# Kernel tuning notes

Measured on AMD Instinct MI355X. Metric: run time of the kernel, lower is better.

The kernel has to match this reference:

```python
import jax, jax.numpy as jnp
import numpy as np

N, E, F_IN, F_EXP, H, C = 8192, 65536, 3247, 7993, 3, 512
HC = H * C
NEG_SLOPE = 0.2


def setup_inputs() -> dict:
    key = jax.random.key(0)
    ks = jax.random.split(key, 40)
    s = 0.02
    rnd = lambda k, *sh: (jax.random.normal(k, sh, jnp.float32) * s)
    d = {}
    d['x'] = jax.random.normal(ks[0], (N, F_IN), jnp.float32)
    d['edge_index'] = jax.random.randint(ks[1], (2, E), 0, N, jnp.int32)
    d['exp'] = jax.random.normal(ks[2], (N, F_EXP), jnp.float32)
    # GATv2 layer 1 (in=3247)
    d['w1l'] = rnd(ks[3], F_IN, HC); d['b1l'] = rnd(ks[4], HC)
    d['w1r'] = rnd(ks[5], F_IN, HC); d['b1r'] = rnd(ks[6], HC)
    d['a1'] = rnd(ks[7], H, C);      d['o1'] = rnd(ks[8], HC)
    # GATv2 layer 2 (in=1536)
    d['w2l'] = rnd(ks[9], HC, HC);  d['b2l'] = rnd(ks[10], HC)
    d['w2r'] = rnd(ks[11], HC, HC); d['b2r'] = rnd(ks[12], HC)
    d['a2'] = rnd(ks[13], H, C);     d['o2'] = rnd(ks[14], HC)
    # GATv2 layer 3 (in=1536)
    d['w3l'] = rnd(ks[15], HC, HC); d['b3l'] = rnd(ks[16], HC)
    d['w3r'] = rnd(ks[17], HC, HC); d['b3r'] = rnd(ks[18], HC)
    d['a3'] = rnd(ks[19], H, C);     d['o3'] = rnd(ks[20], HC)
    # encoder: 7993 -> 4000 -> 1500 -> 512
    d['e1w'] = rnd(ks[21], F_EXP, 4000); d['e1b'] = rnd(ks[22], 4000)
    d['e2w'] = rnd(ks[23], 4000, 1500);  d['e2b'] = rnd(ks[24], 1500)
    d['e3w'] = rnd(ks[25], 1500, 512);   d['e3b'] = rnd(ks[26], 512)
    # head: 2048 -> 1024 -> 512 -> 1
    d['l1w'] = rnd(ks[27], HC + 512, 1024); d['l1b'] = rnd(ks[28], 1024)
    d['l2w'] = rnd(ks[29], 1024, 512);      d['l2b'] = rnd(ks[30], 512)
    d['l3w'] = rnd(ks[31], 512, 1);         d['l3b'] = rnd(ks[32], 1)
    return d


def gatv2(h, src, dst, wl, bl, wr, br, att, out_bias):
    # PyG GATv2Conv: e_ij = a^T LeakyReLU(W_l h_j + W_r h_i), softmax over j per target i,
    # out_i = sum_j alpha_ij * (W_l h_j), concat heads, + bias.
    xl = (h @ wl + bl).reshape(N, H, C)
    xr = (h @ wr + br).reshape(N, H, C)
    e = jax.nn.leaky_relu(xl[src] + xr[dst], NEG_SLOPE)      # [E', H, C]
    logit = jnp.einsum('ehc,hc->eh', e, att)                  # [E', H]
    m = jax.ops.segment_max(logit, dst, num_segments=N)       # [N, H]
    p = jnp.exp(logit - m[dst])
    z = jax.ops.segment_sum(p, dst, num_segments=N)
    alpha = p / z[dst]                                        # segment softmax
    out = jax.ops.segment_sum(alpha[:, :, None] * xl[src], dst, num_segments=N)
    return out.reshape(N, HC) + out_bias


def reference(x, edge_index, exp,
              w1l, b1l, w1r, b1r, a1, o1,
              w2l, b2l, w2r, b2r, a2, o2,
              w3l, b3l, w3r, b3r, a3, o3,
              e1w, e1b, e2w, e2b, e3w, e3b,
              l1w, l1b, l2w, l2b, l3w, l3b):
    loops = jnp.arange(N, dtype=edge_index.dtype)
    src = jnp.concatenate([edge_index[0], loops])  # add_self_loops=True (PyG default)
    dst = jnp.concatenate([edge_index[1], loops])
    h = jax.nn.relu(gatv2(x, src, dst, w1l, b1l, w1r, b1r, a1, o1))
    h = jax.nn.relu(gatv2(h, src, dst, w2l, b2l, w2r, b2r, a2, o2))
    h = jax.nn.relu(gatv2(h, src, dst, w3l, b3l, w3r, b3r, a3, o3))
    cell = jax.nn.relu(exp @ e1w + e1b)
    cell = jax.nn.relu(cell @ e2w + e2b)
    cell = cell @ e3w + e3b
    z = jnp.concatenate([h, cell], axis=1)  # [N, 2048]
    z = jax.nn.relu(z @ l1w + l1b)
    z = jax.nn.relu(z @ l2w + l2b)
    return z @ l3w + l3b  # [N, 1]
```

## Files before the change

kernel.cpp:

```cpp
#include <hip/hip_runtime.h>
#include <stdint.h>

#define NN 8192
#define NE 65536
#define ET (NE + NN)
#define F_IN   3247
#define F_IN_P 3264
#define F_EXP   7993
#define F_EXP_P 8000

typedef __attribute__((ext_vector_type(8))) short bf16x8;
typedef __attribute__((ext_vector_type(4))) float f32x4;

typedef const __attribute__((address_space(1))) void gvoid_t;
typedef __attribute__((address_space(3))) void lvoid_t;

__device__ __forceinline__ float bf2f(uint16_t u) {
  union { uint32_t i; float f; } v; v.i = ((uint32_t)u) << 16; return v.f;
}
__device__ __forceinline__ uint16_t f2bf(float f) {
  union { float f; uint32_t i; } v; v.f = f;
  uint32_t r = v.i + 0x7fffu + ((v.i >> 16) & 1u);
  return (uint16_t)(r >> 16);
}

__device__ __forceinline__ void gld_lds16(const void* g, void* l) {
  __builtin_amdgcn_global_load_lds((gvoid_t*)g, (lvoid_t*)l, 16, 0, 0);
}

#define BARRIER() do { __builtin_amdgcn_sched_barrier(0); \
                       __builtin_amdgcn_s_barrier(); \
                       __builtin_amdgcn_sched_barrier(0); } while (0)
#define LGKM0()   do { asm volatile("s_waitcnt lgkmcnt(0)" ::: "memory"); \
                       __builtin_amdgcn_sched_barrier(0); } while (0)

__device__ __forceinline__ void stage4(const char* src, char* dst, size_t Kb) {
#pragma unroll
  for (int j = 0; j < 4; ++j)
    gld_lds16(src + (size_t)(j * 64) * Kb, dst + j * 8192);
}

__global__ __launch_bounds__(512, 2)
void gemm256(const uint16_t* __restrict__ A, const uint16_t* __restrict__ Bt,
             const float* __restrict__ bias, int biasN, int relu,
             uint16_t* __restrict__ C, int Kp, int ldc, int nbn)
{
  extern __shared__ char smem[];
  const int tid = threadIdx.x;
  const int w = tid >> 6, lane = tid & 63;
  const int wr = w >> 2, wc = w & 3;
  const int fr = lane & 15, g = lane >> 4;

  const int nwg = (int)gridDim.x;
  const int id = (int)blockIdx.x;
  const int q = nwg >> 3, r = nwg & 7;
  const int xcd = id & 7, idx = id >> 3;
  const int wg = (xcd < r ? xcd * (q + 1) : r * (q + 1) + (xcd - r) * q) + idx;
  const int brow = (wg / nbn) * 256, bcol = (wg % nbn) * 256;

  const size_t Kb = (size_t)Kp * 2;

  const int srow = tid >> 3;
  const int sswz = ((tid & 7) ^ (srow & 7)) * 16;
  const char* pA = (const char*)A + (size_t)(brow + srow) * Kb + sswz;
  const char* pB = (const char*)Bt + (size_t)(bcol + srow) * Kb + sswz;
  char* sA = smem + w * 1024;
  char* sB = smem + 65536 + w * 1024;

  const int sw0 = ((g) ^ (fr & 7)) * 16;
  const int sw1 = ((g + 4) ^ (fr & 7)) * 16;
  const int arow = (wr * 128 + fr) * 128;
  const int brow_o = (wc * 64 + fr) * 128;

  f32x4 acc[8][4];
#pragma unroll
  for (int m = 0; m < 8; ++m)
#pragma unroll
    for (int n = 0; n < 4; ++n) acc[m][n] = (f32x4){0.f, 0.f, 0.f, 0.f};
  bf16x8 af[8][2], bg[4][2];

  stage4(pA, sA, Kb);
  stage4(pB, sB, Kb);
  stage4(pA + 128, sA + 32768, Kb);
  stage4(pB + 128, sB + 32768, Kb);
  asm volatile("s_waitcnt vmcnt(8)" ::: "memory");
  BARRIER();

  const int nk = Kp >> 6;
  for (int t = 0; t < nk; ++t) {
    const int buf = (t & 1) << 15;
    const char* aB = smem + buf + arow;
    const char* bB = smem + 65536 + buf + brow_o;

#pragma unroll
    for (int m = 0; m < 4; ++m) {
      af[m][0] = *(const bf16x8*)(aB + m * 2048 + sw0);
      af[m][1] = *(const bf16x8*)(aB + m * 2048 + sw1);
    }
#pragma unroll
    for (int n = 0; n < 2; ++n) {
      bg[n][0] = *(const bf16x8*)(bB + n * 2048 + sw0);
      bg[n][1] = *(const bf16x8*)(bB + n * 2048 + sw1);
    }
    BARRIER(); LGKM0();
    __builtin_amdgcn_s_setprio(1);
#pragma unroll
    for (int m = 0; m < 4; ++m)
#pragma unroll
      for (int n = 0; n < 2; ++n) {
        acc[m][n] = __builtin_amdgcn_mfma_f32_16x16x32_bf16(af[m][0], bg[n][0], acc[m][n], 0, 0, 0);
        acc[m][n] = __builtin_amdgcn_mfma_f32_16x16x32_bf16(af[m][1], bg[n][1], acc[m][n], 0, 0, 0);
      }
    __builtin_amdgcn_s_setprio(0);
    BARRIER();

#pragma unroll
    for (int m = 4; m < 8; ++m) {
      af[m][0] = *(const bf16x8*)(aB + m * 2048 + sw0);
      af[m][1] = *(const bf16x8*)(aB + m * 2048 + sw1);
    }
#pragma unroll
    for (int n = 2; n < 4; ++n) {
      bg[n][0] = *(const bf16x8*)(bB + n * 2048 + sw0);
      bg[n][1] = *(const bf16x8*)(bB + n * 2048 + sw1);
    }
    BARRIER(); LGKM0();
    __builtin_amdgcn_s_setprio(1);
#pragma unroll
    for (int m = 4; m < 8; ++m)
#pragma unroll
      for (int n = 0; n < 2; ++n) {
        acc[m][n] = __builtin_amdgcn_mfma_f32_16x16x32_bf16(af[m][0], bg[n][0], acc[m][n], 0, 0, 0);
        acc[m][n] = __builtin_amdgcn_mfma_f32_16x16x32_bf16(af[m][1], bg[n][1], acc[m][n], 0, 0, 0);
      }
    __builtin_amdgcn_s_setprio(0);
    BARRIER();

    if (t + 2 < nk) stage4(pA + (size_t)(t + 2) * 128, sA + (((t + 2) & 1) << 15), Kb);
    BARRIER();
    __builtin_amdgcn_s_setprio(1);
#pragma unroll
    for (int m = 0; m < 4; ++m)
#pragma unroll
      for (int n = 2; n < 4; ++n) {
        acc[m][n] = __builtin_amdgcn_mfma_f32_16x16x32_bf16(af[m][0], bg[n][0], acc[m][n], 0, 0, 0);
        acc[m][n] = __builtin_amdgcn_mfma_f32_16x16x32_bf16(af[m][1], bg[n][1], acc[m][n], 0, 0, 0);
      }
    __builtin_amdgcn_s_setprio(0);
    BARRIER();

    if (t + 2 < nk) stage4(pB + (size_t)(t + 2) * 128, sB + (((t + 2) & 1) << 15), Kb);
    BARRIER();
    __builtin_amdgcn_s_setprio(1);
#pragma unroll
    for (int m = 4; m < 8; ++m)
#pragma unroll
      for (int n = 2; n < 4; ++n) {
        acc[m][n] = __builtin_amdgcn_mfma_f32_16x16x32_bf16(af[m][0], bg[n][0], acc[m][n], 0, 0, 0);
        acc[m][n] = __builtin_amdgcn_mfma_f32_16x16x32_bf16(af[m][1], bg[n][1], acc[m][n], 0, 0, 0);
      }
    __builtin_amdgcn_s_setprio(0);
    if (t + 2 < nk) { asm volatile("s_waitcnt vmcnt(8)" ::: "memory"); }
    else            { asm volatile("s_waitcnt vmcnt(0)" ::: "memory"); }
    BARRIER();
  }

#pragma unroll
  for (int m = 0; m < 8; ++m) {
    const int row = brow + wr * 128 + m * 16 + g * 4;
#pragma unroll
    for (int n = 0; n < 4; ++n) {
      const int col = bcol + wc * 64 + n * 16 + fr;
      const float bv = (col < biasN) ? bias[col] : 0.f;
#pragma unroll
      for (int j = 0; j < 4; ++j) {
        float v = acc[m][n][j] + bv;
        if (relu) v = fmaxf(v, 0.f);
        C[(size_t)(row + j) * ldc + col] = f2bf(v);
      }
    }
  }
}

__global__ __launch_bounds__(256)
void gemm_bt(const uint16_t* __restrict__ A, const uint16_t* __restrict__ Bt,
             const float* __restrict__ bias, int biasN, int relu,
             uint16_t* __restrict__ C, int Kp, int ldc)
{
  __shared__ uint16_t As[128 * 32];
  __shared__ uint16_t Bs[128 * 32];
  const int tid  = threadIdx.x;
  const int wave = tid >> 6, lane = tid & 63;
  const int brow = blockIdx.x * 128, bcol = blockIdx.y * 128;
  const int wr = wave >> 1, wc = wave & 1;
  const int fr = lane & 15, g = lane >> 4;

  f32x4 acc[4][4];
#pragma unroll
  for (int m = 0; m < 4; ++m)
#pragma unroll
    for (int n = 0; n < 4; ++n) acc[m][n] = (f32x4){0.f, 0.f, 0.f, 0.f};

  const int rA = tid >> 2;
  const int kc = (tid & 3) * 8;
  const uint16_t* aptr = A  + (size_t)(brow + rA) * Kp + kc;
  const uint16_t* bptr = Bt + (size_t)(bcol + rA) * Kp + kc;
  char* ldsA = (char*)As + wave * 1024;
  char* ldsB = (char*)Bs + wave * 1024;
  const size_t rowskip = (size_t)64 * Kp;

  const int nk = Kp >> 5;
  for (int kt = 0; kt < nk; ++kt) {
    __syncthreads();
    gld_lds16(aptr,           ldsA);
    gld_lds16(aptr + rowskip, ldsA + 4096);
    gld_lds16(bptr,           ldsB);
    gld_lds16(bptr + rowskip, ldsB + 4096);
    aptr += 32; bptr += 32;
    __syncthreads();

    bf16x8 af[4], bfr[4];
#pragma unroll
    for (int m = 0; m < 4; ++m)
      af[m] = *(const bf16x8*)&As[(wr * 64 + m * 16 + fr) * 32 + g * 8];
#pragma unroll
    for (int n = 0; n < 4; ++n)
      bfr[n] = *(const bf16x8*)&Bs[(wc * 64 + n * 16 + fr) * 32 + g * 8];
#pragma unroll
    for (int m = 0; m < 4; ++m)
#pragma unroll
      for (int n = 0; n < 4; ++n)
        acc[m][n] = __builtin_amdgcn_mfma_f32_16x16x32_bf16(af[m], bfr[n], acc[m][n], 0, 0, 0);
  }

#pragma unroll
  for (int m = 0; m < 4; ++m) {
    const int row = brow + wr * 64 + m * 16 + g * 4;
#pragma unroll
    for (int n = 0; n < 4; ++n) {
      const int col = bcol + wc * 64 + n * 16 + fr;
      const float bv = (col < biasN) ? bias[col] : 0.f;
#pragma unroll
      for (int j = 0; j < 4; ++j) {
        float v = acc[m][n][j] + bv;
        if (relu) v = fmaxf(v, 0.f);
        C[(size_t)(row + j) * ldc + col] = f2bf(v);
      }
    }
  }
}

__global__ __launch_bounds__(256)
void cvt_pad(const float* __restrict__ in, uint16_t* __restrict__ out, int cols, int colsPad)
{
  const int r = blockIdx.y;
  const int c = (blockIdx.x * 256 + threadIdx.x) * 2;
  if (c >= colsPad) return;
  const float* ip = in + (size_t)r * cols;
  const float v0 = (c < cols)     ? ip[c]     : 0.f;
  const float v1 = (c + 1 < cols) ? ip[c + 1] : 0.f;
  const uint32_t pk = (uint32_t)f2bf(v0) | ((uint32_t)f2bf(v1) << 16);
  *(uint32_t*)(out + (size_t)r * colsPad + c) = pk;
}

__global__ __launch_bounds__(256)
void transpose_w(const float* __restrict__ W, uint16_t* __restrict__ Wt,
                 int K, int N, int Kp, int Np)
{
  __shared__ float t[32][33];
  const int tx = threadIdx.x, ty = threadIdx.y;
  const int k0 = blockIdx.x * 32, n0 = blockIdx.y * 32;
#pragma unroll
  for (int j = 0; j < 4; ++j) {
    const int k = k0 + ty + j * 8, n = n0 + tx;
    t[ty + j * 8][tx] = (k < K && n < N) ? W[(size_t)k * N + n] : 0.f;
  }
  __syncthreads();
#pragma unroll
  for (int j = 0; j < 4; ++j) {
    const int n = n0 + ty + j * 8, k = k0 + tx;
    Wt[(size_t)n * Kp + k] = f2bf(t[tx][ty + j * 8]);
  }
}

__global__ void count_deg(const int* __restrict__ ei, int* __restrict__ counts)
{
  const int e = blockIdx.x * 256 + threadIdx.x;
  if (e >= ET) return;
  const int d = (e < NE) ? ei[NE + e] : (e - NE);
  atomicAdd(&counts[d], 1);
}

__global__ __launch_bounds__(1024)
void scan_deg(const int* __restrict__ counts, int* __restrict__ row_start, int* __restrict__ cursor)
{
  __shared__ int part[1024];
  const int tid = threadIdx.x;
  int loc[8], pre[8], s = 0;
#pragma unroll
  for (int j = 0; j < 8; ++j) { loc[j] = counts[tid * 8 + j]; pre[j] = s; s += loc[j]; }
  part[tid] = s;
  __syncthreads();
  for (int o = 1; o < 1024; o <<= 1) {
    const int v = part[tid];
    const int a = (tid >= o) ? part[tid - o] : 0;
    __syncthreads();
    part[tid] = v + a;
    __syncthreads();
  }
  const int excl = part[tid] - s;
#pragma unroll
  for (int j = 0; j < 8; ++j) {
    const int v = excl + pre[j];
    row_start[tid * 8 + j] = v;
    cursor[tid * 8 + j]    = v;
  }
  if (tid == 1023) row_start[8192] = excl + s;
}

__global__ void scatter_e(const int* __restrict__ ei, int* __restrict__ cursor,
                          int* __restrict__ csr_src, int* __restrict__ csr_dst)
{
  const int e = blockIdx.x * 256 + threadIdx.x;
  if (e >= ET) return;
  const int sx = (e < NE) ? ei[e]      : (e - NE);
  const int d  = (e < NE) ? ei[NE + e] : (e - NE);
  const int pos = atomicAdd(&cursor[d], 1);
  csr_src[pos] = sx;
  csr_dst[pos] = d;
}

__global__ __launch_bounds__(256)
void gat_logits(const uint16_t* __restrict__ xl, const uint16_t* __restrict__ xr,
                const int* __restrict__ csr_src, const int* __restrict__ csr_dst,
                const float* __restrict__ att, float* __restrict__ logit)
{
  const int slot = (blockIdx.x << 2) + (threadIdx.x >> 6);
  if (slot >= ET) return;
  const int lane = threadIdx.x & 63;
  const uint32_t* pl = (const uint32_t*)(xl + (size_t)csr_src[slot] * 1536);
  const uint32_t* pr = (const uint32_t*)(xr + (size_t)csr_dst[slot] * 1536);
  const float2* a2 = (const float2*)att;
  float acc0 = 0.f, acc1 = 0.f, acc2 = 0.f;
#pragma unroll
  for (int it = 0; it < 12; ++it) {
    const int idx = lane + it * 64;
    const uint32_t ul = pl[idx], ur = pr[idx];
    const float2 av = a2[idx];
    float v0 = bf2f((uint16_t)ul)         + bf2f((uint16_t)ur);
    float v1 = bf2f((uint16_t)(ul >> 16)) + bf2f((uint16_t)(ur >> 16));
    v0 = v0 > 0.f ? v0 : 0.2f * v0;
    v1 = v1 > 0.f ? v1 : 0.2f * v1;
    const float p = v0 * av.x + v1 * av.y;
    if (it < 4) acc0 += p; else if (it < 8) acc1 += p; else acc2 += p;
  }
#pragma unroll
  for (int o = 32; o; o >>= 1) {
    acc0 += __shfl_xor(acc0, o);
    acc1 += __shfl_xor(acc1, o);
    acc2 += __shfl_xor(acc2, o);
  }
  if (lane == 0) {
    float* op = logit + (size_t)slot * 3;
    op[0] = acc0; op[1] = acc1; op[2] = acc2;
  }
}

__global__ __launch_bounds__(256)
void gat_aggregate(const float* __restrict__ logit, const int* __restrict__ csr_src,
                   const int* __restrict__ row_start, const uint16_t* __restrict__ xl,
                   const float* __restrict__ ob, uint16_t* __restrict__ out, int ldc)
{
  const int i = blockIdx.x;
  const int tid = threadIdx.x;
  const int s0 = row_start[i], s1 = row_start[i + 1];

  float m0 = -1e30f, m1 = -1e30f, m2 = -1e30f, z0 = 0.f, z1 = 0.f, z2 = 0.f;
  for (int s = s0; s < s1; ++s) {
    const float* lp = logit + (size_t)s * 3;
    float l0 = lp[0], l1 = lp[1], l2 = lp[2];
    float n0 = fmaxf(m0, l0); z0 = z0 * __expf(m0 - n0) + __expf(l0 - n0); m0 = n0;
    float n1 = fmaxf(m1, l1); z1 = z1 * __expf(m1 - n1) + __expf(l1 - n1); m1 = n1;
    float n2 = fmaxf(m2, l2); z2 = z2 * __expf(m2 - n2) + __expf(l2 - n2); m2 = n2;
  }
  const float r0 = 1.f / z0, r1 = 1.f / z1, r2 = 1.f / z2;

  float acc[6] = {0.f, 0.f, 0.f, 0.f, 0.f, 0.f};
  for (int s = s0; s < s1; ++s) {
    const float* lp = logit + (size_t)s * 3;
    const float w0 = __expf(lp[0] - m0) * r0;
    const float w1 = __expf(lp[1] - m1) * r1;
    const float w2 = __expf(lp[2] - m2) * r2;
    const uint16_t* px = xl + (size_t)csr_src[s] * 1536;
    acc[0] += w0 * bf2f(px[tid]);        acc[1] += w0 * bf2f(px[tid + 256]);
    acc[2] += w1 * bf2f(px[tid + 512]);  acc[3] += w1 * bf2f(px[tid + 768]);
    acc[4] += w2 * bf2f(px[tid + 1024]); acc[5] += w2 * bf2f(px[tid + 1280]);
  }
#pragma unroll
  for (int j = 0; j < 6; ++j) {
    const int c = tid + j * 256;
    float v = acc[j] + ob[c];
    v = fmaxf(v, 0.f);
    out[(size_t)i * ldc + c] = f2bf(v);
  }
}

__global__ __launch_bounds__(256)
void final_dot(const uint16_t* __restrict__ z2, const float* __restrict__ w,
               const float* __restrict__ b, float* __restrict__ out)
{
  const int row  = blockIdx.x * 4 + (threadIdx.x >> 6);
  const int lane = threadIdx.x & 63;
  const uint16_t* p = z2 + (size_t)row * 512;
  float s = 0.f;
#pragma unroll
  for (int j = 0; j < 8; ++j) { const int c = lane + j * 64; s += bf2f(p[c]) * w[c]; }
#pragma unroll
  for (int o = 32; o; o >>= 1) s += __shfl_xor(s, o);
  if (lane == 0) out[row] = s + b[0];
}

extern "C" void kernel_launch(void* const* d_in, const int* in_sizes, int n_in,
                              void* d_out, int out_size, void* d_ws, size_t ws_size,
                              hipStream_t stream)
{
  (void)in_sizes; (void)n_in; (void)out_size; (void)ws_size;

  const float* x    = (const float*)d_in[0];
  const int*   ei   = (const int*)  d_in[1];
  const float* expm = (const float*)d_in[2];
  const float* w1l = (const float*)d_in[3];  const float* b1l = (const float*)d_in[4];
  const float* w1r = (const float*)d_in[5];  const float* b1r = (const float*)d_in[6];
  const float* a1  = (const float*)d_in[7];  const float* o1  = (const float*)d_in[8];
  const float* w2l = (const float*)d_in[9];  const float* b2l = (const float*)d_in[10];
  const float* w2r = (const float*)d_in[11]; const float* b2r = (const float*)d_in[12];
  const float* a2  = (const float*)d_in[13]; const float* o2  = (const float*)d_in[14];
  const float* w3l = (const float*)d_in[15]; const float* b3l = (const float*)d_in[16];
  const float* w3r = (const float*)d_in[17]; const float* b3r = (const float*)d_in[18];
  const float* a3  = (const float*)d_in[19]; const float* o3  = (const float*)d_in[20];
  const float* e1w = (const float*)d_in[21]; const float* e1b = (const float*)d_in[22];
  const float* e2w = (const float*)d_in[23]; const float* e2b = (const float*)d_in[24];
  const float* e3w = (const float*)d_in[25]; const float* e3b = (const float*)d_in[26];
  const float* l1w = (const float*)d_in[27]; const float* l1b = (const float*)d_in[28];
  const float* l2w = (const float*)d_in[29]; const float* l2b = (const float*)d_in[30];
  const float* l3w = (const float*)d_in[31]; const float* l3b = (const float*)d_in[32];
  float* out = (float*)d_out;

  hipFuncSetAttribute((const void*)gemm256, hipFuncAttributeMaxDynamicSharedMemorySize, 131072);

  char* ws = (char*)d_ws;
  size_t off = 0;
  auto take = [&](size_t b) { char* p = ws + off; off += (b + 255) & ~(size_t)255; return p; };

  int*      counts    = (int*)take((size_t)NN * 4);
  int*      row_start = (int*)take((size_t)(NN + 1) * 4);
  int*      cursor    = (int*)take((size_t)NN * 4);
  int*      csr_src   = (int*)take((size_t)ET * 4);
  int*      csr_dst   = (int*)take((size_t)ET * 4);
  float*    logits    = (float*)take((size_t)ET * 3 * 4);
  uint16_t* zbuf      = (uint16_t*)take((size_t)NN * 2048 * 2);
  char*     regA      = take((size_t)NN * F_EXP_P * 2);
  char*     regW      = take((size_t)4096 * F_EXP_P * 2);
  char*     regC      = take((size_t)NN * 4096 * 2 + (size_t)NN * 1536 * 2);

  const size_t HCB = (size_t)NN * 1536 * 2;
  uint16_t* xbf   = (uint16_t*)regA;
  uint16_t* expbf = (uint16_t*)regA;
  uint16_t* wT    = (uint16_t*)regW;
  uint16_t* xlb   = (uint16_t*)regC;
  uint16_t* xrb   = (uint16_t*)(regC + HCB);
  uint16_t* hbuf  = (uint16_t*)(regC + 2 * HCB);
  uint16_t* cell1 = (uint16_t*)regC;
  uint16_t* cell2 = (uint16_t*)(regC + (size_t)NN * 4096 * 2);
  uint16_t* zz1   = (uint16_t*)regC;
  uint16_t* zz2   = (uint16_t*)(regC + (size_t)NN * 1024 * 2);

  hipMemsetAsync(counts, 0, (size_t)NN * 4, stream);
  count_deg<<<(ET + 255) / 256, 256, 0, stream>>>(ei, counts);
  scan_deg<<<1, 1024, 0, stream>>>(counts, row_start, cursor);
  scatter_e<<<(ET + 255) / 256, 256, 0, stream>>>(ei, cursor, csr_src, csr_dst);

  cvt_pad<<<dim3((F_IN_P / 2 + 255) / 256, NN), 256, 0, stream>>>(x, xbf, F_IN, F_IN_P);
  transpose_w<<<dim3(F_IN_P / 32, 1536 / 32), dim3(32, 8), 0, stream>>>(w1l, wT, F_IN, 1536, F_IN_P, 1536);
  gemm256<<<32 * 6, 512, 131072, stream>>>(xbf, wT, b1l, 1536, 0, xlb, F_IN_P, 1536, 6);
  transpose_w<<<dim3(F_IN_P / 32, 1536 / 32), dim3(32, 8), 0, stream>>>(w1r, wT, F_IN, 1536, F_IN_P, 1536);
  gemm256<<<32 * 6, 512, 131072, stream>>>(xbf, wT, b1r, 1536, 0, xrb, F_IN_P, 1536, 6);
  gat_logits<<<ET / 4, 256, 0, stream>>>(xlb, xrb, csr_src, csr_dst, a1, logits);
  gat_aggregate<<<NN, 256, 0, stream>>>(logits, csr_src, row_start, xlb, o1, hbuf, 1536);

  transpose_w<<<dim3(48, 48), dim3(32, 8), 0, stream>>>(w2l, wT, 1536, 1536, 1536, 1536);
  gemm256<<<32 * 6, 512, 131072, stream>>>(hbuf, wT, b2l, 1536, 0, xlb, 1536, 1536, 6);
  transpose_w<<<dim3(48, 48), dim3(32, 8), 0, stream>>>(w2r, wT, 1536, 1536, 1536, 1536);
  gemm256<<<32 * 6, 512, 131072, stream>>>(hbuf, wT, b2r, 1536, 0, xrb, 1536, 1536, 6);
  gat_logits<<<ET / 4, 256, 0, stream>>>(xlb, xrb, csr_src, csr_dst, a2, logits);
  gat_aggregate<<<NN, 256, 0, stream>>>(logits, csr_src, row_start, xlb, o2, hbuf, 1536);

  transpose_w<<<dim3(48, 48), dim3(32, 8), 0, stream>>>(w3l, wT, 1536, 1536, 1536, 1536);
  gemm256<<<32 * 6, 512, 131072, stream>>>(hbuf, wT, b3l, 1536, 0, xlb, 1536, 1536, 6);
  transpose_w<<<dim3(48, 48), dim3(32, 8), 0, stream>>>(w3r, wT, 1536, 1536, 1536, 1536);
  gemm256<<<32 * 6, 512, 131072, stream>>>(hbuf, wT, b3r, 1536, 0, xrb, 1536, 1536, 6);
  gat_logits<<<ET / 4, 256, 0, stream>>>(xlb, xrb, csr_src, csr_dst, a3, logits);
  gat_aggregate<<<NN, 256, 0, stream>>>(logits, csr_src, row_start, xlb, o3, zbuf, 2048);

  cvt_pad<<<dim3((F_EXP_P / 2 + 255) / 256, NN), 256, 0, stream>>>(expm, expbf, F_EXP, F_EXP_P);
  transpose_w<<<dim3(F_EXP_P / 32, 4096 / 32), dim3(32, 8), 0, stream>>>(e1w, wT, F_EXP, 4000, F_EXP_P, 4096);
  gemm256<<<32 * 16, 512, 131072, stream>>>(expbf, wT, e1b, 4000, 1, cell1, F_EXP_P, 4096, 16);
  transpose_w<<<dim3(4096 / 32, 1536 / 32), dim3(32, 8), 0, stream>>>(e2w, wT, 4000, 1500, 4096, 1536);
  gemm256<<<32 * 6, 512, 131072, stream>>>(cell1, wT, e2b, 1500, 1, cell2, 4096, 1536, 6);
  transpose_w<<<dim3(1536 / 32, 512 / 32), dim3(32, 8), 0, stream>>>(e3w, wT, 1500, 512, 1536, 512);
  gemm_bt<<<dim3(64, 4), 256, 0, stream>>>(cell2, wT, e3b, 512, 0, zbuf + 1536, 1536, 2048);

  transpose_w<<<dim3(2048 / 32, 1024 / 32), dim3(32, 8), 0, stream>>>(l1w, wT, 2048, 1024, 2048, 1024);
  gemm_bt<<<dim3(64, 8), 256, 0, stream>>>(zbuf, wT, l1b, 1024, 1, zz1, 2048, 1024);
  transpose_w<<<dim3(1024 / 32, 512 / 32), dim3(32, 8), 0, stream>>>(l2w, wT, 1024, 512, 1024, 512);
  gemm_bt<<<dim3(64, 4), 256, 0, stream>>>(zz1, wT, l2b, 512, 1, zz2, 1024, 512);
  final_dot<<<NN / 4, 256, 0, stream>>>(zz2, l3w, l3b, out);
}
```

Measured before the change: 1.699 ms.

## Software-pipeline LDS fragment loads across quadrants in gemm256 and use it for head layer

```diff
diff --git a/kernel.cpp b/kernel.cpp
--- a/kernel.cpp
+++ b/kernel.cpp
@@ -28,11 +28,9 @@
   __builtin_amdgcn_global_load_lds((gvoid_t*)g, (lvoid_t*)l, 16, 0, 0);
 }
 
-#define BARRIER() do { __builtin_amdgcn_sched_barrier(0); \
-                       __builtin_amdgcn_s_barrier(); \
-                       __builtin_amdgcn_sched_barrier(0); } while (0)
-#define LGKM0()   do { asm volatile("s_waitcnt lgkmcnt(0)" ::: "memory"); \
-                       __builtin_amdgcn_sched_barrier(0); } while (0)
+#define SBAR() __builtin_amdgcn_sched_barrier(0)
+#define BARRIER() do { SBAR(); __builtin_amdgcn_s_barrier(); SBAR(); } while (0)
+#define MFMA16(a, b, c) __builtin_amdgcn_mfma_f32_16x16x32_bf16(a, b, c, 0, 0, 0)
 
 __device__ __forceinline__ void stage4(const char* src, char* dst, size_t Kb) {
 #pragma unroll
@@ -67,7 +65,7 @@
   char* sA = smem + w * 1024;
   char* sB = smem + 65536 + w * 1024;
 
-  const int sw0 = ((g) ^ (fr & 7)) * 16;
+  const int sw0 = (g ^ (fr & 7)) * 16;
   const int sw1 = ((g + 4) ^ (fr & 7)) * 16;
   const int arow = (wr * 128 + fr) * 128;
   const int brow_o = (wc * 64 + fr) * 128;
@@ -77,7 +75,7 @@
   for (int m = 0; m < 8; ++m)
 #pragma unroll
     for (int n = 0; n < 4; ++n) acc[m][n] = (f32x4){0.f, 0.f, 0.f, 0.f};
-  bf16x8 af[8][2], bg[4][2];
+  bf16x8 a03[8], a47[8], b01[4], b23[4];
 
   stage4(pA, sA, Kb);
   stage4(pB, sB, Kb);
@@ -85,83 +83,108 @@
   stage4(pB + 128, sB + 32768, Kb);
   asm volatile("s_waitcnt vmcnt(8)" ::: "memory");
   BARRIER();
+  {
+    const char* aB = smem + arow;
+    const char* bB = smem + 65536 + brow_o;
+#pragma unroll
+    for (int m = 0; m < 4; ++m) {
+      a03[m * 2]     = *(const bf16x8*)(aB + m * 2048 + sw0);
+      a03[m * 2 + 1] = *(const bf16x8*)(aB + m * 2048 + sw1);
+    }
+#pragma unroll
+    for (int n = 0; n < 2; ++n) {
+      b01[n * 2]     = *(const bf16x8*)(bB + n * 2048 + sw0);
+      b01[n * 2 + 1] = *(const bf16x8*)(bB + n * 2048 + sw1);
+    }
+  }
+  SBAR();
 
   const int nk = Kp >> 6;
   for (int t = 0; t < nk; ++t) {
     const int buf = (t & 1) << 15;
-    const char* aB = smem + buf + arow;
-    const char* bB = smem + 65536 + buf + brow_o;
+    const int nbuf = buf ^ 32768;
+    const char* aB  = smem + buf + arow;
+    const char* bB  = smem + 65536 + buf + brow_o;
+    const char* aBn = smem + nbuf + arow;
+    const char* bBn = smem + 65536 + nbuf + brow_o;
+    const bool nls = (t + 2 < nk);
+    const bool nlr = (t + 1 < nk);
 
 #pragma unroll
     for (int m = 0; m < 4; ++m) {
-      af[m][0] = *(const bf16x8*)(aB + m * 2048 + sw0);
-      af[m][1] = *(const bf16x8*)(aB + m * 2048 + sw1);
-    }
-#pragma unroll
-    for (int n = 0; n < 2; ++n) {
-      bg[n][0] = *(const bf16x8*)(bB + n * 2048 + sw0);
-      bg[n][1] = *(const bf16x8*)(bB + n * 2048 + sw1);
-    }
-    BARRIER(); LGKM0();
+      a47[m * 2]     = *(const bf16x8*)(aB + (m + 4) * 2048 + sw0);
+      a47[m * 2 + 1] = *(const bf16x8*)(aB + (m + 4) * 2048 + sw1);
+    }
+    SBAR();
     __builtin_amdgcn_s_setprio(1);
 #pragma unroll
     for (int m = 0; m < 4; ++m)
 #pragma unroll
       for (int n = 0; n < 2; ++n) {
-        acc[m][n] = __builtin_amdgcn_mfma_f32_16x16x32_bf16(af[m][0], bg[n][0], acc[m][n], 0, 0, 0);
-        acc[m][n] = __builtin_amdgcn_mfma_f32_16x16x32_bf16(af[m][1], bg[n][1], acc[m][n], 0, 0, 0);
+        acc[m][n] = MFMA16(a03[m * 2],     b01[n * 2],     acc[m][n]);
+        acc[m][n] = MFMA16(a03[m * 2 + 1], b01[n * 2 + 1], acc[m][n]);
       }
     __builtin_amdgcn_s_setprio(0);
     BARRIER();
 
 #pragma unroll
-    for (int m = 4; m < 8; ++m) {
-      af[m][0] = *(const bf16x8*)(aB + m * 2048 + sw0);
-      af[m][1] = *(const bf16x8*)(aB + m * 2048 + sw1);
-    }
-#pragma unroll
-    for (int n = 2; n < 4; ++n) {
-      bg[n][0] = *(const bf16x8*)(bB + n * 2048 + sw0);
-      bg[n][1] = *(const bf16x8*)(bB + n * 2048 + sw1);
-    }
-    BARRIER(); LGKM0();
+    for (int n = 0; n < 2; ++n) {
+      b23[n * 2]     = *(const bf16x8*)(bB + (n + 2) * 2048 + sw0);
+      b23[n * 2 + 1] = *(const bf16x8*)(bB + (n + 2) * 2048 + sw1);
+    }
+    SBAR();
     __builtin_amdgcn_s_setprio(1);
 #pragma unroll
-    for (int m = 4; m < 8; ++m)
+    for (int m = 0; m < 4; ++m)
 #pragma unroll
       for (int n = 0; n < 2; ++n) {
-        acc[m][n] = __builtin_amdgcn_mfma_f32_16x16x32_bf16(af[m][0], bg[n][0], acc[m][n], 0, 0, 0);
-        acc[m][n] = __builtin_amdgcn_mfma_f32_16x16x32_bf16(af[m][1], bg[n][1], acc[m][n], 0, 0, 0);
+        acc[m + 4][n] = MFMA16(a47[m * 2],     b01[n * 2],     acc[m + 4][n]);
+        acc[m + 4][n] = MFMA16(a47[m * 2 + 1], b01[n * 2 + 1], acc[m + 4][n]);
       }
     __builtin_amdgcn_s_setprio(0);
     BARRIER();
 
-    if (t + 2 < nk) stage4(pA + (size_t)(t + 2) * 128, sA + (((t + 2) & 1) << 15), Kb);
-    BARRIER();
+    if (nls) {
+      stage4(pA + (size_t)(t + 2) * 128, sA + buf, Kb);
+      asm volatile("s_waitcnt vmcnt(4)" ::: "memory");
+    } else {
+      asm volatile("s_waitcnt vmcnt(0)" ::: "memory");
+    }
+    SBAR();
     __builtin_amdgcn_s_setprio(1);
 #pragma unroll
     for (int m = 0; m < 4; ++m)
 #pragma unroll
-      for (int n = 2; n < 4; ++n) {
-        acc[m][n] = __builtin_amdgcn_mfma_f32_16x16x32_bf16(af[m][0], bg[n][0], acc[m][n], 0, 0, 0);
-        acc[m][n] = __builtin_amdgcn_mfma_f32_16x16x32_bf16(af[m][1], bg[n][1], acc[m][n], 0, 0, 0);
+      for (int n = 0; n < 2; ++n) {
+        acc[m][n + 2] = MFMA16(a03[m * 2],     b23[n * 2],     acc[m][n + 2]);
+        acc[m][n + 2] = MFMA16(a03[m * 2 + 1], b23[n * 2 + 1], acc[m][n + 2]);
       }
     __builtin_amdgcn_s_setprio(0);
     BARRIER();
 
-    if (t + 2 < nk) stage4(pB + (size_t)(t + 2) * 128, sB + (((t + 2) & 1) << 15), Kb);
-    BARRIER();
+    if (nlr) {
+#pragma unroll
+      for (int m = 0; m < 4; ++m) {
+        a03[m * 2]     = *(const bf16x8*)(aBn + m * 2048 + sw0);
+        a03[m * 2 + 1] = *(const bf16x8*)(aBn + m * 2048 + sw1);
+      }
+#pragma unroll
+      for (int n = 0; n < 2; ++n) {
+        b01[n * 2]     = *(const bf16x8*)(bBn + n * 2048 + sw0);
+        b01[n * 2 + 1] = *(const bf16x8*)(bBn + n * 2048 + sw1);
+      }
+    }
+    if (nls) stage4(pB + (size_t)(t + 2) * 128, sB + buf, Kb);
+    SBAR();
     __builtin_amdgcn_s_setprio(1);
 #pragma unroll
-    for (int m = 4; m < 8; ++m)
-#pragma unroll
-      for (int n = 2; n < 4; ++n) {
-        acc[m][n] = __builtin_amdgcn_mfma_f32_16x16x32_bf16(af[m][0], bg[n][0], acc[m][n], 0, 0, 0);
-        acc[m][n] = __builtin_amdgcn_mfma_f32_16x16x32_bf16(af[m][1], bg[n][1], acc[m][n], 0, 0, 0);
+    for (int m = 0; m < 4; ++m)
+#pragma unroll
+      for (int n = 0; n < 2; ++n) {
+        acc[m + 4][n + 2] = MFMA16(a47[m * 2],     b23[n * 2],     acc[m + 4][n + 2]);
+        acc[m + 4][n + 2] = MFMA16(a47[m * 2 + 1], b23[n * 2 + 1], acc[m + 4][n + 2]);
       }
     __builtin_amdgcn_s_setprio(0);
-    if (t + 2 < nk) { asm volatile("s_waitcnt vmcnt(8)" ::: "memory"); }
-    else            { asm volatile("s_waitcnt vmcnt(0)" ::: "memory"); }
     BARRIER();
   }
 
@@ -230,7 +253,7 @@
     for (int m = 0; m < 4; ++m)
 #pragma unroll
       for (int n = 0; n < 4; ++n)
-        acc[m][n] = __builtin_amdgcn_mfma_f32_16x16x32_bf16(af[m], bfr[n], acc[m][n], 0, 0, 0);
+        acc[m][n] = MFMA16(af[m], bfr[n], acc[m][n]);
   }
 
 #pragma unroll
@@ -511,7 +534,7 @@
   gemm_bt<<<dim3(64, 4), 256, 0, stream>>>(cell2, wT, e3b, 512, 0, zbuf + 1536, 1536, 2048);
 
   transpose_w<<<dim3(2048 / 32, 1024 / 32), dim3(32, 8), 0, stream>>>(l1w, wT, 2048, 1024, 2048, 1024);
-  gemm_bt<<<dim3(64, 8), 256, 0, stream>>>(zbuf, wT, l1b, 1024, 1, zz1, 2048, 1024);
+  gemm256<<<32 * 4, 512, 131072, stream>>>(zbuf, wT, l1b, 1024, 1, zz1, 2048, 1024, 4);
   transpose_w<<<dim3(1024 / 32, 512 / 32), dim3(32, 8), 0, stream>>>(l2w, wT, 1024, 512, 1024, 512);
   gemm_bt<<<dim3(64, 4), 256, 0, stream>>>(zz1, wT, l2b, 512, 1, zz2, 1024, 512);
   final_dot<<<NN / 4, 256, 0, stream>>>(zz2, l3w, l3b, out);
```

Result: slower. 2.161 ms (+27.2%).
